# Optimization experiments

Measured on AMD Instinct MI355X. Metric: run time of the kernel, lower is better.

## Reference

```python
import jax, jax.numpy as jnp
import numpy as np

N = 100000   # nodes
E = 1600000  # edges (avg degree 16)
F = 128      # num_node_features
H = 128      # hid_size
G = 512      # num graphs in batch
C = 10       # num_classes
D = 32       # graph_degree_distribution.shape[1]
BN_EPS = 1e-5


def setup_inputs() -> dict:
    key = jax.random.key(0)
    ks = jax.random.split(key, 16)
    p = lambda k, shp: jax.random.normal(k, shp, jnp.float32) * 0.02
    x = jax.random.normal(ks[0], (N, F), jnp.float32)
    edge_index = jax.random.randint(ks[1], (2, E), 0, N)
    batch = jnp.sort(jax.random.randint(ks[2], (N,), 0, G))
    degree = jax.random.uniform(ks[3], (N,), jnp.float32) * 10.0
    return dict(
        x=x, edge_index=edge_index, batch=batch, degree=degree,
        eps1=jnp.zeros(()), W1a=p(ks[4], (F, H)), b1a=jnp.zeros(H), W1b=p(ks[5], (H, H)), b1b=jnp.zeros(H),
        g1=jnp.ones(H), be1=jnp.zeros(H),
        eps2=jnp.zeros(()), W2a=p(ks[6], (H, H)), b2a=jnp.zeros(H), W2b=p(ks[7], (H, H)), b2b=jnp.zeros(H),
        g2=jnp.ones(H), be2=jnp.zeros(H),
        Wlin1=p(ks[8], (H, H)), blin1=jnp.zeros(H),
        Wlin2=p(ks[9], (H, C)), blin2=jnp.zeros(C),
        Wlin4=p(ks[10], (H, D)), blin4=jnp.zeros(D),
        Wloss=p(ks[11], (H, 1)), bloss=jnp.zeros(1),
    )


def gin_conv(x, src, dst, eps, Wa, ba, Wb, bb, gamma, beta):
    # GINConv: MLP((1+eps)*x_i + sum_{j->i} x_j); MLP = Lin-ReLU-Lin-ReLU-BN
    agg = jax.ops.segment_sum(x[src], dst, num_segments=x.shape[0])  # [N,F] gather-scatter
    h = (1.0 + eps) * x + agg
    h = jax.nn.relu(h @ Wa + ba)
    h = jax.nn.relu(h @ Wb + bb)
    mu = h.mean(0)
    var = h.var(0)  # biased var, training-mode BN
    return gamma * (h - mu) * jax.lax.rsqrt(var + BN_EPS) + beta


def reference(x, edge_index, batch, degree,
              eps1, W1a, b1a, W1b, b1b, g1, be1,
              eps2, W2a, b2a, W2b, b2b, g2, be2,
              Wlin1, blin1, Wlin2, blin2, Wlin4, blin4, Wloss, bloss):
    src, dst = edge_index[0], edge_index[1]
    h = gin_conv(x, src, dst, eps1, W1a, b1a, W1b, b1b, g1, be1)
    h = gin_conv(h, src, dst, eps2, W2a, b2a, W2b, b2b, g2, be2)
    mse_x = h @ Wloss + bloss                       # [N,1]
    mse_loss = jnp.mean((mse_x - degree[:, None]) ** 2)
    # global_mean_pool over graphs
    sums = jax.ops.segment_sum(h, batch, num_segments=G)
    cnts = jax.ops.segment_sum(jnp.ones((h.shape[0], 1), h.dtype), batch, num_segments=G)
    g = sums / jnp.maximum(cnts, 1.0)               # [G,H]
    z = jax.nn.relu(g @ Wlin1 + blin1)              # dropout inert (eval)
    result1 = jax.nn.log_softmax(z @ Wlin2 + blin2, axis=-1)  # [G,C]
    result3 = z @ Wlin4 + blin4                      # [G,D]
    return result1, result3, mse_loss
```

## Files before the change

kernel.cpp:

```cpp
#include <hip/hip_runtime.h>
#include <hip/hip_bf16.h>

#define HF 128
#define BSH 8
#define BSZ 256
#define NBMAX 1024
#define FCAP 8192
#define AST 136
#define HB 512

typedef __attribute__((ext_vector_type(8))) short bf16x8;
typedef __attribute__((ext_vector_type(4))) float f32x4;
typedef __attribute__((ext_vector_type(2))) float f32x2;

__device__ inline float bflo(unsigned u) { return __uint_as_float(u << 16); }
__device__ inline float bfhi(unsigned u) { return __uint_as_float(u & 0xffff0000u); }
__device__ inline unsigned short f2bf(float f) {
    unsigned u = __float_as_uint(f);
    unsigned r = (u + 0x7fffu + ((u >> 16) & 1u)) >> 16;
    return (unsigned short)r;
}
__device__ inline unsigned pack2(float a, float b) {
    return (unsigned)f2bf(a) | ((unsigned)f2bf(b) << 16);
}
__device__ inline uint2 pk8_fp8(const float* v) {
    int a = __builtin_amdgcn_cvt_pk_fp8_f32(v[0], v[1], 0, 0);
    a = __builtin_amdgcn_cvt_pk_fp8_f32(v[2], v[3], a, 1);
    int b = __builtin_amdgcn_cvt_pk_fp8_f32(v[4], v[5], 0, 0);
    b = __builtin_amdgcn_cvt_pk_fp8_f32(v[6], v[7], b, 1);
    uint2 r; r.x = (unsigned)a; r.y = (unsigned)b;
    return r;
}

__global__ __launch_bounds__(256) void init_all(
    const float* __restrict__ x, unsigned short* __restrict__ xb,
    unsigned char* __restrict__ x8, int castBlk, int nchunks,
    const float* __restrict__ w0, const float* __restrict__ w1,
    const float* __restrict__ w2, const float* __restrict__ w3,
    unsigned short* __restrict__ WtAll,
    const int* __restrict__ dst, int* __restrict__ bpart, int E, int chunkH,
    const int* __restrict__ batch, int* __restrict__ gstart, int N, int Gn, int nBlocks,
    float* __restrict__ Szero, float* __restrict__ outm)
{
    __shared__ int lh[NBMAX];
    int b = blockIdx.x;
    int t = threadIdx.x;
    if (b < castBlk) {
        int i = b * 256 + t;
        if (i < nchunks) {
            float4 a = ((const float4*)x)[2 * i];
            float4 c = ((const float4*)x)[2 * i + 1];
            uint4 o;
            o.x = pack2(a.x, a.y); o.y = pack2(a.z, a.w);
            o.z = pack2(c.x, c.y); o.w = pack2(c.z, c.w);
            ((uint4*)xb)[i] = o;
            float v[8] = {a.x, a.y, a.z, a.w, c.x, c.y, c.z, c.w};
            ((uint2*)x8)[i] = pk8_fp8(v);
        }
        return;
    }
    b -= castBlk;
    if (b < 4) {
        const float* W = (b == 0) ? w0 : (b == 1) ? w1 : (b == 2) ? w2 : w3;
        unsigned short* O = WtAll + b * 16384;
        for (int idx = t; idx < 16384; idx += 256) {
            int n = idx >> 7, k = idx & 127;
            O[idx] = f2bf(W[k * 128 + n]);
        }
        return;
    }
    b -= 4;
    if (b < HB) {
        int NBl = (N + BSZ - 1) >> BSH;
        for (int i = t; i < NBl; i += 256) lh[i] = 0;
        __syncthreads();
        int beg = b * chunkH;
        int end = min(E, beg + chunkH);
        for (int e = beg + t; e < end; e += 256)
            atomicAdd(&lh[dst[e] >> BSH], 1);
        __syncthreads();
        for (int i = t; i < NBl; i += 256) bpart[i * HB + b] = lh[i];
        return;
    }
    b -= HB;
    if (b < nBlocks) {
        int i = b * 256 + t;
        if (i >= N) return;
        int bi = batch[i];
        int bp = (i == 0) ? -1 : batch[i - 1];
        for (int g = bp + 1; g <= bi; g++) gstart[g] = i;
        if (i == N - 1)
            for (int g = bi + 1; g <= Gn; g++) gstart[g] = N;
        return;
    }
    if (t < 2 * HF) { Szero[t] = 0.f; Szero[t + 2 * HF] = 0.f; }
    if (t == 0) outm[0] = 0.f;
}

__global__ void scanp(const int* __restrict__ bpart, int* __restrict__ boff,
                      int* __restrict__ bcur, int NB, int E)
{
    __shared__ int tot[NBMAX];
    __shared__ int part[256];
    int t = threadIdx.x;
    for (int i = t; i < NB; i += 256) {
        const int4* pp = (const int4*)(bpart + (size_t)i * HB);
        int run = 0;
#pragma unroll 4
        for (int b = 0; b < HB / 4; b++) {
            int4 v = pp[b];
            run += v.x + v.y + v.z + v.w;
        }
        tot[i] = run;
    }
    __syncthreads();
    int v[4];
    int s = 0;
#pragma unroll
    for (int i = 0; i < 4; i++) {
        int idx = t * 4 + i;
        v[i] = (idx < NB) ? tot[idx] : 0;
        s += v[i];
    }
    part[t] = s;
    __syncthreads();
    for (int o = 1; o < 256; o <<= 1) {
        int y = (t >= o) ? part[t - o] : 0;
        __syncthreads();
        part[t] += y;
        __syncthreads();
    }
    int base = part[t] - s;
#pragma unroll
    for (int i = 0; i < 4; i++) {
        int idx = t * 4 + i;
        if (idx < NB) { boff[idx] = base; bcur[idx] = base; base += v[i]; }
    }
    if (t == 0) boff[NB] = E;
}

__global__ __launch_bounds__(256) void bucket_bin(
    const int* __restrict__ src, const int* __restrict__ dst,
    int* __restrict__ bcur, unsigned* __restrict__ ebuf, int E, int NB, int chunkH)
{
    __shared__ int lh[NBMAX];
    int t = threadIdx.x;
    for (int i = t; i < NB; i += 256) lh[i] = 0;
    __syncthreads();
    int beg = blockIdx.x * chunkH;
    int end = min(E, beg + chunkH);
    for (int e = beg + t; e < end; e += 256)
        atomicAdd(&lh[dst[e] >> BSH], 1);
    __syncthreads();
    for (int i = t; i < NB; i += 256) {
        int c = lh[i];
        lh[i] = c ? atomicAdd(&bcur[i], c) : 0;
    }
    __syncthreads();
    for (int e = beg + t; e < end; e += 256) {
        int d = dst[e];
        int b = d >> BSH;
        int pos = atomicAdd(&lh[b], 1);
        ebuf[pos] = ((unsigned)src[e] << BSH) | (unsigned)(d & (BSZ - 1));
    }
}

__global__ __launch_bounds__(256) void bucket_fill(
    const unsigned* __restrict__ ebuf, const int* __restrict__ boff,
    int* __restrict__ off, int* __restrict__ esrc, int N, int NB, int E)
{
    __shared__ int deg[BSZ];
    __shared__ int pref[BSZ];
    __shared__ int lcur[BSZ];
    __shared__ int lsr[FCAP];
    int b = blockIdx.x;
    int t = threadIdx.x;
    int segBeg = boff[b], segEnd = boff[b + 1];
    int segLen = segEnd - segBeg;
    int node0 = b << BSH;
    deg[t] = 0;
    __syncthreads();
    for (int i = segBeg + t; i < segEnd; i += 256)
        atomicAdd(&deg[ebuf[i] & (BSZ - 1)], 1);
    __syncthreads();
    int dv = deg[t];
    pref[t] = dv;
    __syncthreads();
    for (int o = 1; o < 256; o <<= 1) {
        int y = (t >= o) ? pref[t - o] : 0;
        __syncthreads();
        pref[t] += y;
        __syncthreads();
    }
    int excl = pref[t] - dv;
    int node = node0 + t;
    if (node < N) off[node] = segBeg + excl;
    lcur[t] = excl;
    if (b == NB - 1 && t == 0) off[N] = E;
    __syncthreads();
    if (segLen <= FCAP) {
        for (int i = segBeg + t; i < segEnd; i += 256) {
            unsigned v = ebuf[i];
            int slot = atomicAdd(&lcur[v & (BSZ - 1)], 1);
            lsr[slot] = (int)(v >> BSH);
        }
        __syncthreads();
        for (int i = t; i < segLen; i += 256) esrc[segBeg + i] = lsr[i];
    } else {
        for (int i = segBeg + t; i < segEnd; i += 256) {
            unsigned v = ebuf[i];
            int slot = atomicAdd(&lcur[v & (BSZ - 1)], 1);
            esrc[segBeg + slot] = (int)(v >> BSH);
        }
    }
}

template <bool FOLD>
__global__ __launch_bounds__(256) void gather_u(
    const unsigned short* __restrict__ xb, const unsigned char* __restrict__ x8,
    const int* __restrict__ off, const int* __restrict__ esrc,
    const float* __restrict__ epsp,
    const float* __restrict__ S1, const float* __restrict__ S2,
    const float* __restrict__ gamma, const float* __restrict__ beta, float invN,
    unsigned short* __restrict__ Uo, int N)
{
    __shared__ float lsc[HF], lsh[HF];
    int tid = threadIdx.x;
    if (FOLD) {
        if (tid < HF) {
            float mu = S1[tid] * invN;
            float var = S2[tid] * invN - mu * mu;
            float rs = rsqrtf(var + 1e-5f);
            float sc = gamma[tid] * rs;
            lsc[tid] = sc;
            lsh[tid] = beta[tid] - mu * sc;
        }
        __syncthreads();
    }
    int lane16 = tid & 15;
    int node = (blockIdx.x * 256 + tid) >> 4;
    if (node >= N) return;
    int beg = off[node], end = off[node + 1];
    float acc[8] = {0.f, 0.f, 0.f, 0.f, 0.f, 0.f, 0.f, 0.f};
    for (int j0 = beg; j0 < end; j0 += 16) {
        int myidx = (j0 + lane16 < end) ? esrc[j0 + lane16] : 0;
        int cnt = min(16, end - j0);
        for (int t = 0; t < cnt; t++) {
            int s = __shfl(myidx, t, 16);
            uint2 p = *(const uint2*)(x8 + (size_t)s * HF + lane16 * 8);
            f32x2 f0 = __builtin_amdgcn_cvt_pk_f32_fp8((int)p.x, 0);
            f32x2 f1 = __builtin_amdgcn_cvt_pk_f32_fp8((int)p.x, 1);
            f32x2 f2 = __builtin_amdgcn_cvt_pk_f32_fp8((int)p.y, 0);
            f32x2 f3 = __builtin_amdgcn_cvt_pk_f32_fp8((int)p.y, 1);
            acc[0] += f0.x; acc[1] += f0.y;
            acc[2] += f1.x; acc[3] += f1.y;
            acc[4] += f2.x; acc[5] += f2.y;
            acc[6] += f3.x; acc[7] += f3.y;
        }
    }
    float ep = 1.0f + epsp[0];
    uint4 xx = *(const uint4*)(xb + (size_t)node * HF + lane16 * 8);
    acc[0] += ep * bflo(xx.x); acc[1] += ep * bfhi(xx.x);
    acc[2] += ep * bflo(xx.y); acc[3] += ep * bfhi(xx.y);
    acc[4] += ep * bflo(xx.z); acc[5] += ep * bfhi(xx.z);
    acc[6] += ep * bflo(xx.w); acc[7] += ep * bfhi(xx.w);
    if (FOLD) {
        float cf = ep + (float)(end - beg);
        const float4 s0 = *(const float4*)(&lsc[lane16 * 8]);
        const float4 s1 = *(const float4*)(&lsc[lane16 * 8 + 4]);
        const float4 h0 = *(const float4*)(&lsh[lane16 * 8]);
        const float4 h1 = *(const float4*)(&lsh[lane16 * 8 + 4]);
        acc[0] = acc[0] * s0.x + h0.x * cf; acc[1] = acc[1] * s0.y + h0.y * cf;
        acc[2] = acc[2] * s0.z + h0.z * cf; acc[3] = acc[3] * s0.w + h0.w * cf;
        acc[4] = acc[4] * s1.x + h1.x * cf; acc[5] = acc[5] * s1.y + h1.y * cf;
        acc[6] = acc[6] * s1.z + h1.z * cf; acc[7] = acc[7] * s1.w + h1.w * cf;
    }
    uint4 o;
    o.x = pack2(acc[0], acc[1]); o.y = pack2(acc[2], acc[3]);
    o.z = pack2(acc[4], acc[5]); o.w = pack2(acc[6], acc[7]);
    *(uint4*)(Uo + (size_t)node * HF + lane16 * 8) = o;
}

__global__ __launch_bounds__(256) void gemm2L(
    const unsigned short* __restrict__ U,
    const unsigned short* __restrict__ Wta, const float* __restrict__ ba,
    const unsigned short* __restrict__ Wtb, const float* __restrict__ bb,
    unsigned short* __restrict__ out, unsigned char* __restrict__ out8,
    float* __restrict__ S1, float* __restrict__ S2, int n)
{
    __shared__ unsigned short lW[128 * AST];
    __shared__ unsigned short lT[64 * AST];
    __shared__ float lS1[HF], lS2[HF];
    int tid = threadIdx.x;
    int w = tid >> 6, lane = tid & 63;
    int m = lane & 15, quad = lane >> 4;
    int row0 = blockIdx.x * 64;
    if (tid < HF) { lS1[tid] = 0.f; lS2[tid] = 0.f; }

    for (int c = tid; c < 2048; c += 256) {
        int r = c >> 4, k16 = c & 15;
        *(uint4*)(&lW[r * AST + k16 * 8]) = *(const uint4*)(Wta + r * HF + k16 * 8);
    }
    __syncthreads();

    int arow = row0 + w * 16 + m;
    if (arow >= n) arow = n - 1;
    bf16x8 aF[4];
#pragma unroll
    for (int kk = 0; kk < 4; kk++)
        aF[kk] = *(const bf16x8*)(U + (size_t)arow * HF + kk * 32 + quad * 8);

    f32x4 acc[8];
#pragma unroll
    for (int nt = 0; nt < 8; nt++) acc[nt] = (f32x4){0.f, 0.f, 0.f, 0.f};
#pragma unroll
    for (int nt = 0; nt < 8; nt++) {
#pragma unroll
        for (int kk = 0; kk < 4; kk++) {
            bf16x8 b = *(const bf16x8*)(&lW[(nt * 16 + m) * AST + kk * 32 + quad * 8]);
            acc[nt] = __builtin_amdgcn_mfma_f32_16x16x32_bf16(aF[kk], b, acc[nt], 0, 0, 0);
        }
    }
#pragma unroll
    for (int nt = 0; nt < 8; nt++) {
        float bav = ba[nt * 16 + m];
#pragma unroll
        for (int r = 0; r < 4; r++) {
            int lrow = w * 16 + quad * 4 + r;
            lT[lrow * AST + nt * 16 + m] = f2bf(fmaxf(acc[nt][r] + bav, 0.f));
        }
    }
    __syncthreads();
    for (int c = tid; c < 2048; c += 256) {
        int r = c >> 4, k16 = c & 15;
        *(uint4*)(&lW[r * AST + k16 * 8]) = *(const uint4*)(Wtb + r * HF + k16 * 8);
    }
    __syncthreads();

#pragma unroll
    for (int kk = 0; kk < 4; kk++)
        aF[kk] = *(const bf16x8*)(&lT[(w * 16 + m) * AST + kk * 32 + quad * 8]);
#pragma unroll
    for (int nt = 0; nt < 8; nt++) acc[nt] = (f32x4){0.f, 0.f, 0.f, 0.f};
#pragma unroll
    for (int nt = 0; nt < 8; nt++) {
#pragma unroll
        for (int kk = 0; kk < 4; kk++) {
            bf16x8 b = *(const bf16x8*)(&lW[(nt * 16 + m) * AST + kk * 32 + quad * 8]);
            acc[nt] = __builtin_amdgcn_mfma_f32_16x16x32_bf16(aF[kk], b, acc[nt], 0, 0, 0);
        }
    }
#pragma unroll
    for (int nt = 0; nt < 8; nt++) {
        int col = nt * 16 + m;
        float bbv = bb[col];
        float cs = 0.f, cq = 0.f;
#pragma unroll
        for (int r = 0; r < 4; r++) {
            int lrow = w * 16 + quad * 4 + r;
            int grow = row0 + lrow;
            float v = fmaxf(acc[nt][r] + bbv, 0.f);
            lT[lrow * AST + col] = f2bf(v);
            if (grow < n) { cs += v; cq += v * v; }
        }
        cs += __shfl_down(cs, 32); cs += __shfl_down(cs, 16);
        cq += __shfl_down(cq, 32); cq += __shfl_down(cq, 16);
        if (quad == 0) { atomicAdd(&lS1[col], cs); atomicAdd(&lS2[col], cq); }
    }
#pragma unroll
    for (int i = 0; i < 4; i++) {
        int idx = i * 64 + lane;
        int r = idx >> 4, k16 = idx & 15;
        int grow = row0 + w * 16 + r;
        if (grow < n) {
            uint4 v = *(const uint4*)(&lT[(w * 16 + r) * AST + k16 * 8]);
            *(uint4*)(out + (size_t)grow * HF + k16 * 8) = v;
            if (out8) {
                float f[8] = {bflo(v.x), bfhi(v.x), bflo(v.y), bfhi(v.y),
                              bflo(v.z), bfhi(v.z), bflo(v.w), bfhi(v.w)};
                *(uint2*)(out8 + (size_t)grow * HF + k16 * 8) = pk8_fp8(f);
            }
        }
    }
    __syncthreads();
    if (tid < HF) { atomicAdd(&S1[tid], lS1[tid]); atomicAdd(&S2[tid], lS2[tid]); }
}

__global__ __launch_bounds__(512) void pool_tail(
    const unsigned short* __restrict__ h2raw,
    const float* __restrict__ S1, const float* __restrict__ S2,
    const float* __restrict__ gamma, const float* __restrict__ beta, float invN,
    const int* __restrict__ gstart, const float* __restrict__ W,
    const float* __restrict__ bias,
    const float* __restrict__ Wloss, const float* __restrict__ blossp,
    const float* __restrict__ degree,
    const float* __restrict__ W2, const float* __restrict__ b2,
    const float* __restrict__ W4, const float* __restrict__ b4,
    float* __restrict__ out1, float* __restrict__ out3,
    float* __restrict__ outm, int C_, int D_)
{
    __shared__ float lsc[HF], lsh[HF];
    __shared__ float red[8][HF];
    __shared__ float gv[HF];
    __shared__ float part[4][HF];
    __shared__ float wred[8];
    __shared__ float zz[HF];
    __shared__ float logits[16];
    __shared__ float lse_s;
    int gid = blockIdx.x;
    int t = threadIdx.x;
    if (t < HF) {
        float mu = S1[t] * invN;
        float var = S2[t] * invN - mu * mu;
        float rs = rsqrtf(var + 1e-5f);
        float sc = gamma[t] * rs;
        lsc[t] = sc;
        lsh[t] = beta[t] - mu * sc;
    }
    __syncthreads();
    int c2 = t & 63;
    int rg = t >> 6;
    int b = gstart[gid], e = gstart[gid + 1];
    float wla = lsc[2 * c2] * Wloss[2 * c2];
    float wlb = lsc[2 * c2 + 1] * Wloss[2 * c2 + 1];
    float c0l = lsh[2 * c2] * Wloss[2 * c2] + lsh[2 * c2 + 1] * Wloss[2 * c2 + 1];
    float bl = blossp[0];
    float s0 = 0.f, s1 = 0.f, macc = 0.f;
    for (int r = b + rg; r < e; r += 8) {
        unsigned u = *(const unsigned*)(h2raw + (size_t)r * HF + c2 * 2);
        float v0 = bflo(u), v1 = bfhi(u);
        s0 += v0; s1 += v1;
        float m = v0 * wla + v1 * wlb + c0l;
#pragma unroll
        for (int o = 32; o > 0; o >>= 1) m += __shfl_down(m, o);
        if (c2 == 0) {
            float d = m + bl - degree[r];
            macc += d * d;
        }
    }
    red[rg][c2 * 2] = s0;
    red[rg][c2 * 2 + 1] = s1;
    if (c2 == 0) wred[rg] = macc;
    __syncthreads();
    if (t < HF) {
        float s = red[0][t] + red[1][t] + red[2][t] + red[3][t]
                + red[4][t] + red[5][t] + red[6][t] + red[7][t];
        gv[t] = (e > b) ? lsc[t] * (s / (float)(e - b)) + lsh[t] : 0.f;
    }
    __syncthreads();
    int c = t & 127, kg = t >> 7;
    float a = 0.f;
#pragma unroll 8
    for (int k = kg * 32; k < kg * 32 + 32; k++) a += gv[k] * W[(size_t)k * HF + c];
    part[kg][c] = a;
    __syncthreads();
    if (t < HF) {
        float aa = part[0][t] + part[1][t] + part[2][t] + part[3][t] + bias[t];
        zz[t] = fmaxf(aa, 0.f);
    }
    if (t == 0) {
        float ps = wred[0] + wred[1] + wred[2] + wred[3]
                 + wred[4] + wred[5] + wred[6] + wred[7];
        atomicAdd(outm, ps * invN);
    }
    __syncthreads();
    if (t < C_) {
        float aa = b2[t];
        for (int k = 0; k < HF; k++) aa += zz[k] * W2[(size_t)k * C_ + t];
        logits[t] = aa;
    }
    __syncthreads();
    if (t == 0) {
        float mx = -1e30f;
        for (int i = 0; i < C_; i++) mx = fmaxf(mx, logits[i]);
        float s = 0.f;
        for (int i = 0; i < C_; i++) s += expf(logits[i] - mx);
        lse_s = mx + logf(s);
    }
    __syncthreads();
    if (t < C_) out1[(size_t)gid * C_ + t] = logits[t] - lse_s;
    if (t < D_) {
        float aa = b4[t];
        for (int k = 0; k < HF; k++) aa += zz[k] * W4[(size_t)k * D_ + t];
        out3[(size_t)gid * D_ + t] = aa;
    }
}

extern "C" void kernel_launch(void* const* d_in, const int* in_sizes, int n_in,
                              void* d_out, int out_size, void* d_ws, size_t ws_size,
                              hipStream_t stream)
{
    const float* x      = (const float*)d_in[0];
    const int*   ei     = (const int*)d_in[1];
    const int*   batch  = (const int*)d_in[2];
    const float* degree = (const float*)d_in[3];
    const float* eps1   = (const float*)d_in[4];
    const float* W1a    = (const float*)d_in[5];
    const float* b1a    = (const float*)d_in[6];
    const float* W1b    = (const float*)d_in[7];
    const float* b1b    = (const float*)d_in[8];
    const float* g1     = (const float*)d_in[9];
    const float* be1    = (const float*)d_in[10];
    const float* eps2   = (const float*)d_in[11];
    const float* W2a    = (const float*)d_in[12];
    const float* b2a    = (const float*)d_in[13];
    const float* W2b    = (const float*)d_in[14];
    const float* b2b    = (const float*)d_in[15];
    const float* g2     = (const float*)d_in[16];
    const float* be2    = (const float*)d_in[17];
    const float* Wlin1  = (const float*)d_in[18];
    const float* blin1  = (const float*)d_in[19];
    const float* Wlin2  = (const float*)d_in[20];
    const float* blin2  = (const float*)d_in[21];
    const float* Wlin4  = (const float*)d_in[22];
    const float* blin4  = (const float*)d_in[23];
    const float* Wloss  = (const float*)d_in[24];
    const float* bloss  = (const float*)d_in[25];

    const int N  = in_sizes[0] / HF;
    const int E  = in_sizes[1] / 2;
    const int C_ = in_sizes[21];
    const int D_ = in_sizes[23];
    const int Gn = (out_size - 1) / (C_ + D_);
    const int NB = (N + BSZ - 1) >> BSH;

    const int* src = ei;
    const int* dst = ei + E;

    size_t NH = (size_t)N * HF;
    char* p = (char*)d_ws;
    unsigned short* xb  = (unsigned short*)p; p += NH * 2;
    unsigned short* U   = (unsigned short*)p; p += NH * 2;
    unsigned short* Hp1 = (unsigned short*)p; p += NH * 2;
    unsigned short* Hp2 = (unsigned short*)p; p += NH * 2;
    unsigned char*  x8  = (unsigned char*)p; p += NH;
    unsigned char*  h8  = (unsigned char*)p; p += NH;
    unsigned short* WtAll = (unsigned short*)p; p += 4 * 16384 * 2;
    float* S1a  = (float*)p; p += HF * 4;
    float* S2a  = (float*)p; p += HF * 4;
    float* S1b  = (float*)p; p += HF * 4;
    float* S2b  = (float*)p; p += HF * 4;
    int* gstart = (int*)p; p += (Gn + 1) * 4;
    int* boff   = (int*)p; p += (NBMAX + 1) * 4;
    int* bcur   = (int*)p; p += NBMAX * 4;
    int* bpart  = (int*)p; p += (size_t)NBMAX * HB * 4;
    int* off    = (int*)p; p += (N + 1) * 4;
    int* esrc   = (int*)p; p += E * 4;
    unsigned* ebuf = (unsigned*)p; p += E * 4;

    unsigned short* Wt1a = WtAll;
    unsigned short* Wt1b = WtAll + 16384;
    unsigned short* Wt2a = WtAll + 32768;
    unsigned short* Wt2b = WtAll + 49152;

    float* out1 = (float*)d_out;
    float* out3 = out1 + (size_t)Gn * C_;
    float* outm = out3 + (size_t)Gn * D_;

    int nchunks  = (int)(NH / 8);
    int castBlk  = (nchunks + 255) / 256;
    int nBlocks  = (N + 255) / 256;
    int gatherBlk = (N * 16 + 255) / 256;
    int gemmBlk  = (N + 63) / 64;
    int chunkH   = (E + HB - 1) / HB;
    float invN = 1.0f / (float)N;

    int initBlk = castBlk + 4 + HB + nBlocks + 1;

    init_all<<<initBlk, 256, 0, stream>>>(x, xb, x8, castBlk, nchunks,
                                          W1a, W1b, W2a, W2b, WtAll,
                                          dst, bpart, E, chunkH,
                                          batch, gstart, N, Gn, nBlocks,
                                          S1a, outm);
    scanp<<<1, 256, 0, stream>>>(bpart, boff, bcur, NB, E);
    bucket_bin<<<HB, 256, 0, stream>>>(src, dst, bcur, ebuf, E, NB, chunkH);
    bucket_fill<<<NB, 256, 0, stream>>>(ebuf, boff, off, esrc, N, NB, E);
    gather_u<false><<<gatherBlk, 256, 0, stream>>>(xb, x8, off, esrc, eps1,
                                                   nullptr, nullptr, nullptr, nullptr, 0.f, U, N);
    gemm2L<<<gemmBlk, 256, 0, stream>>>(U, Wt1a, b1a, Wt1b, b1b, Hp1, h8, S1a, S2a, N);
    gather_u<true><<<gatherBlk, 256, 0, stream>>>(Hp1, h8, off, esrc, eps2,
                                                  S1a, S2a, g1, be1, invN, U, N);
    gemm2L<<<gemmBlk, 256, 0, stream>>>(U, Wt2a, b2a, Wt2b, b2b, Hp2, nullptr, S1b, S2b, N);
    pool_tail<<<Gn, 512, 0, stream>>>(Hp2, S1b, S2b, g2, be2, invN, gstart,
                                      Wlin1, blin1, Wloss, bloss, degree,
                                      Wlin2, blin2, Wlin4, blin4,
                                      out1, out3, outm, C_, D_);
}
```

Before: 466.6 us.

## Switch GIN MLP GEMMs and intermediates to FP8 MFMA

Weights are now stored as FP8. The aggregated features U are written as FP8 instead of bf16, and both linear layers in each GIN MLP use the fp8 16x16x32 MFMA. The layer-1 bf16 output Hp1 is dropped, and the second gather reads its self term from the FP8 copy. The aim is to cut memory traffic and LDS footprint and to raise MFMA throughput, at the cost of noticeably lower numerical precision, including FP8 quantization of the hidden activations between the two linears.

```diff
diff --git a/kernel.cpp b/kernel.cpp
--- a/kernel.cpp
+++ b/kernel.cpp
@@ -7,6 +7,7 @@
 #define NBMAX 1024
 #define FCAP 8192
 #define AST 136
+#define WST 136
 #define HB 512
 
 typedef __attribute__((ext_vector_type(8))) short bf16x8;
@@ -31,13 +32,16 @@
     uint2 r; r.x = (unsigned)a; r.y = (unsigned)b;
     return r;
 }
+__device__ inline long long u2ll(uint2 q) {
+    return (long long)(((unsigned long long)q.y << 32) | (unsigned long long)q.x);
+}
 
 __global__ __launch_bounds__(256) void init_all(
     const float* __restrict__ x, unsigned short* __restrict__ xb,
     unsigned char* __restrict__ x8, int castBlk, int nchunks,
     const float* __restrict__ w0, const float* __restrict__ w1,
     const float* __restrict__ w2, const float* __restrict__ w3,
-    unsigned short* __restrict__ WtAll,
+    unsigned char* __restrict__ Wt8All,
     const int* __restrict__ dst, int* __restrict__ bpart, int E, int chunkH,
     const int* __restrict__ batch, int* __restrict__ gstart, int N, int Gn, int nBlocks,
     float* __restrict__ Szero, float* __restrict__ outm)
@@ -62,10 +66,12 @@
     b -= castBlk;
     if (b < 4) {
         const float* W = (b == 0) ? w0 : (b == 1) ? w1 : (b == 2) ? w2 : w3;
-        unsigned short* O = WtAll + b * 16384;
+        unsigned char* O = Wt8All + b * 16384;
         for (int idx = t; idx < 16384; idx += 256) {
             int n = idx >> 7, k = idx & 127;
-            O[idx] = f2bf(W[k * 128 + n]);
+            float wv = W[k * 128 + n];
+            int r = __builtin_amdgcn_cvt_pk_fp8_f32(wv, wv, 0, 0);
+            O[idx] = (unsigned char)(r & 0xff);
         }
         return;
     }
@@ -222,7 +228,7 @@
     const float* __restrict__ epsp,
     const float* __restrict__ S1, const float* __restrict__ S2,
     const float* __restrict__ gamma, const float* __restrict__ beta, float invN,
-    unsigned short* __restrict__ Uo, int N)
+    unsigned char* __restrict__ U8, int N)
 {
     __shared__ float lsc[HF], lsh[HF];
     int tid = threadIdx.x;
@@ -259,12 +265,16 @@
         }
     }
     float ep = 1.0f + epsp[0];
-    uint4 xx = *(const uint4*)(xb + (size_t)node * HF + lane16 * 8);
-    acc[0] += ep * bflo(xx.x); acc[1] += ep * bfhi(xx.x);
-    acc[2] += ep * bflo(xx.y); acc[3] += ep * bfhi(xx.y);
-    acc[4] += ep * bflo(xx.z); acc[5] += ep * bfhi(xx.z);
-    acc[6] += ep * bflo(xx.w); acc[7] += ep * bfhi(xx.w);
     if (FOLD) {
+        uint2 sp = *(const uint2*)(x8 + (size_t)node * HF + lane16 * 8);
+        f32x2 f0 = __builtin_amdgcn_cvt_pk_f32_fp8((int)sp.x, 0);
+        f32x2 f1 = __builtin_amdgcn_cvt_pk_f32_fp8((int)sp.x, 1);
+        f32x2 f2 = __builtin_amdgcn_cvt_pk_f32_fp8((int)sp.y, 0);
+        f32x2 f3 = __builtin_amdgcn_cvt_pk_f32_fp8((int)sp.y, 1);
+        acc[0] += ep * f0.x; acc[1] += ep * f0.y;
+        acc[2] += ep * f1.x; acc[3] += ep * f1.y;
+        acc[4] += ep * f2.x; acc[5] += ep * f2.y;
+        acc[6] += ep * f3.x; acc[7] += ep * f3.y;
         float cf = ep + (float)(end - beg);
         const float4 s0 = *(const float4*)(&lsc[lane16 * 8]);
         const float4 s1 = *(const float4*)(&lsc[lane16 * 8 + 4]);
@@ -274,21 +284,25 @@
         acc[2] = acc[2] * s0.z + h0.z * cf; acc[3] = acc[3] * s0.w + h0.w * cf;
         acc[4] = acc[4] * s1.x + h1.x * cf; acc[5] = acc[5] * s1.y + h1.y * cf;
         acc[6] = acc[6] * s1.z + h1.z * cf; acc[7] = acc[7] * s1.w + h1.w * cf;
-    }
-    uint4 o;
-    o.x = pack2(acc[0], acc[1]); o.y = pack2(acc[2], acc[3]);
-    o.z = pack2(acc[4], acc[5]); o.w = pack2(acc[6], acc[7]);
-    *(uint4*)(Uo + (size_t)node * HF + lane16 * 8) = o;
-}
-
-__global__ __launch_bounds__(256) void gemm2L(
-    const unsigned short* __restrict__ U,
-    const unsigned short* __restrict__ Wta, const float* __restrict__ ba,
-    const unsigned short* __restrict__ Wtb, const float* __restrict__ bb,
+    } else {
+        uint4 xx = *(const uint4*)(xb + (size_t)node * HF + lane16 * 8);
+        acc[0] += ep * bflo(xx.x); acc[1] += ep * bfhi(xx.x);
+        acc[2] += ep * bflo(xx.y); acc[3] += ep * bfhi(xx.y);
+        acc[4] += ep * bflo(xx.z); acc[5] += ep * bfhi(xx.z);
+        acc[6] += ep * bflo(xx.w); acc[7] += ep * bfhi(xx.w);
+    }
+    *(uint2*)(U8 + (size_t)node * HF + lane16 * 8) = pk8_fp8(acc);
+}
+
+template <bool EMIT_BF16>
+__global__ __launch_bounds__(256) void gemm2F(
+    const unsigned char* __restrict__ U8,
+    const unsigned char* __restrict__ Wt8a, const float* __restrict__ ba,
+    const unsigned char* __restrict__ Wt8b, const float* __restrict__ bb,
     unsigned short* __restrict__ out, unsigned char* __restrict__ out8,
     float* __restrict__ S1, float* __restrict__ S2, int n)
 {
-    __shared__ unsigned short lW[128 * AST];
+    __shared__ unsigned char lW[128 * WST];
     __shared__ unsigned short lT[64 * AST];
     __shared__ float lS1[HF], lS2[HF];
     int tid = threadIdx.x;
@@ -297,18 +311,18 @@
     int row0 = blockIdx.x * 64;
     if (tid < HF) { lS1[tid] = 0.f; lS2[tid] = 0.f; }
 
-    for (int c = tid; c < 2048; c += 256) {
-        int r = c >> 4, k16 = c & 15;
-        *(uint4*)(&lW[r * AST + k16 * 8]) = *(const uint4*)(Wta + r * HF + k16 * 8);
-    }
-    __syncthreads();
-
     int arow = row0 + w * 16 + m;
     if (arow >= n) arow = n - 1;
-    bf16x8 aF[4];
+    long long aF[4];
 #pragma unroll
     for (int kk = 0; kk < 4; kk++)
-        aF[kk] = *(const bf16x8*)(U + (size_t)arow * HF + kk * 32 + quad * 8);
+        aF[kk] = *(const long long*)(U8 + (size_t)arow * HF + kk * 32 + quad * 8);
+
+    for (int c = tid; c < 2048; c += 256) {
+        int r = c >> 4, k8 = c & 15;
+        *(uint2*)(&lW[r * WST + k8 * 8]) = *(const uint2*)(Wt8a + r * HF + k8 * 8);
+    }
+    __syncthreads();
 
     f32x4 acc[8];
 #pragma unroll
@@ -317,8 +331,8 @@
     for (int nt = 0; nt < 8; nt++) {
 #pragma unroll
         for (int kk = 0; kk < 4; kk++) {
-            bf16x8 b = *(const bf16x8*)(&lW[(nt * 16 + m) * AST + kk * 32 + quad * 8]);
-            acc[nt] = __builtin_amdgcn_mfma_f32_16x16x32_bf16(aF[kk], b, acc[nt], 0, 0, 0);
+            long long b = *(const long long*)(&lW[(nt * 16 + m) * WST + kk * 32 + quad * 8]);
+            acc[nt] = __builtin_amdgcn_mfma_f32_16x16x32_fp8_fp8(aF[kk], b, acc[nt], 0, 0, 0);
         }
     }
 #pragma unroll
@@ -332,22 +346,26 @@
     }
     __syncthreads();
     for (int c = tid; c < 2048; c += 256) {
-        int r = c >> 4, k16 = c & 15;
-        *(uint4*)(&lW[r * AST + k16 * 8]) = *(const uint4*)(Wtb + r * HF + k16 * 8);
-    }
-    __syncthreads();
-
-#pragma unroll
-    for (int kk = 0; kk < 4; kk++)
-        aF[kk] = *(const bf16x8*)(&lT[(w * 16 + m) * AST + kk * 32 + quad * 8]);
+        int r = c >> 4, k8 = c & 15;
+        *(uint2*)(&lW[r * WST + k8 * 8]) = *(const uint2*)(Wt8b + r * HF + k8 * 8);
+    }
+    __syncthreads();
+
+#pragma unroll
+    for (int kk = 0; kk < 4; kk++) {
+        uint4 tv = *(const uint4*)(&lT[(w * 16 + m) * AST + kk * 32 + quad * 8]);
+        float f[8] = {bflo(tv.x), bfhi(tv.x), bflo(tv.y), bfhi(tv.y),
+                      bflo(tv.z), bfhi(tv.z), bflo(tv.w), bfhi(tv.w)};
+        aF[kk] = u2ll(pk8_fp8(f));
+    }
 #pragma unroll
     for (int nt = 0; nt < 8; nt++) acc[nt] = (f32x4){0.f, 0.f, 0.f, 0.f};
 #pragma unroll
     for (int nt = 0; nt < 8; nt++) {
 #pragma unroll
         for (int kk = 0; kk < 4; kk++) {
-            bf16x8 b = *(const bf16x8*)(&lW[(nt * 16 + m) * AST + kk * 32 + quad * 8]);
-            acc[nt] = __builtin_amdgcn_mfma_f32_16x16x32_bf16(aF[kk], b, acc[nt], 0, 0, 0);
+            long long b = *(const long long*)(&lW[(nt * 16 + m) * WST + kk * 32 + quad * 8]);
+            acc[nt] = __builtin_amdgcn_mfma_f32_16x16x32_fp8_fp8(aF[kk], b, acc[nt], 0, 0, 0);
         }
     }
 #pragma unroll
@@ -374,8 +392,9 @@
         int grow = row0 + w * 16 + r;
         if (grow < n) {
             uint4 v = *(const uint4*)(&lT[(w * 16 + r) * AST + k16 * 8]);
-            *(uint4*)(out + (size_t)grow * HF + k16 * 8) = v;
-            if (out8) {
+            if (EMIT_BF16) {
+                *(uint4*)(out + (size_t)grow * HF + k16 * 8) = v;
+            } else {
                 float f[8] = {bflo(v.x), bfhi(v.x), bflo(v.y), bfhi(v.y),
                               bflo(v.z), bfhi(v.z), bflo(v.w), bfhi(v.w)};
                 *(uint2*)(out8 + (size_t)grow * HF + k16 * 8) = pk8_fp8(f);
@@ -530,12 +549,11 @@
     size_t NH = (size_t)N * HF;
     char* p = (char*)d_ws;
     unsigned short* xb  = (unsigned short*)p; p += NH * 2;
-    unsigned short* U   = (unsigned short*)p; p += NH * 2;
-    unsigned short* Hp1 = (unsigned short*)p; p += NH * 2;
     unsigned short* Hp2 = (unsigned short*)p; p += NH * 2;
+    unsigned char*  U8  = (unsigned char*)p; p += NH;
     unsigned char*  x8  = (unsigned char*)p; p += NH;
     unsigned char*  h8  = (unsigned char*)p; p += NH;
-    unsigned short* WtAll = (unsigned short*)p; p += 4 * 16384 * 2;
+    unsigned char*  Wt8All = (unsigned char*)p; p += 4 * 16384;
     float* S1a  = (float*)p; p += HF * 4;
     float* S2a  = (float*)p; p += HF * 4;
     float* S1b  = (float*)p; p += HF * 4;
@@ -548,10 +566,10 @@
     int* esrc   = (int*)p; p += E * 4;
     unsigned* ebuf = (unsigned*)p; p += E * 4;
 
-    unsigned short* Wt1a = WtAll;
-    unsigned short* Wt1b = WtAll + 16384;
-    unsigned short* Wt2a = WtAll + 32768;
-    unsigned short* Wt2b = WtAll + 49152;
+    unsigned char* Wt8_1a = Wt8All;
+    unsigned char* Wt8_1b = Wt8All + 16384;
+    unsigned char* Wt8_2a = Wt8All + 32768;
+    unsigned char* Wt8_2b = Wt8All + 49152;
 
     float* out1 = (float*)d_out;
     float* out3 = out1 + (size_t)Gn * C_;
@@ -568,7 +586,7 @@
     int initBlk = castBlk + 4 + HB + nBlocks + 1;
 
     init_all<<<initBlk, 256, 0, stream>>>(x, xb, x8, castBlk, nchunks,
-                                          W1a, W1b, W2a, W2b, WtAll,
+                                          W1a, W1b, W2a, W2b, Wt8All,
                                           dst, bpart, E, chunkH,
                                           batch, gstart, N, Gn, nBlocks,
                                           S1a, outm);
@@ -576,11 +594,13 @@
     bucket_bin<<<HB, 256, 0, stream>>>(src, dst, bcur, ebuf, E, NB, chunkH);
     bucket_fill<<<NB, 256, 0, stream>>>(ebuf, boff, off, esrc, N, NB, E);
     gather_u<false><<<gatherBlk, 256, 0, stream>>>(xb, x8, off, esrc, eps1,
-                                                   nullptr, nullptr, nullptr, nullptr, 0.f, U, N);
-    gemm2L<<<gemmBlk, 256, 0, stream>>>(U, Wt1a, b1a, Wt1b, b1b, Hp1, h8, S1a, S2a, N);
-    gather_u<true><<<gatherBlk, 256, 0, stream>>>(Hp1, h8, off, esrc, eps2,
-                                                  S1a, S2a, g1, be1, invN, U, N);
-    gemm2L<<<gemmBlk, 256, 0, stream>>>(U, Wt2a, b2a, Wt2b, b2b, Hp2, nullptr, S1b, S2b, N);
+                                                   nullptr, nullptr, nullptr, nullptr, 0.f, U8, N);
+    gemm2F<false><<<gemmBlk, 256, 0, stream>>>(U8, Wt8_1a, b1a, Wt8_1b, b1b,
+                                               nullptr, h8, S1a, S2a, N);
+    gather_u<true><<<gatherBlk, 256, 0, stream>>>(nullptr, h8, off, esrc, eps2,
+                                                  S1a, S2a, g1, be1, invN, U8, N);
+    gemm2F<true><<<gemmBlk, 256, 0, stream>>>(U8, Wt8_2a, b2a, Wt8_2b, b2b,
+                                              Hp2, nullptr, S1b, S2b, N);
     pool_tail<<<Gn, 512, 0, stream>>>(Hp2, S1b, S2b, g2, be2, invN, gstart,
                                       Wlin1, blin1, Wloss, bloss, degree,
                                       Wlin2, blin2, Wlin4, blin4,
```

Result: no change. 467.8 us (+0.3%).
